# Kernel tuning notes

Hardware: AMD Instinct MI355X
Metric: run time of the kernel (lower is better)

The kernel has to match this reference:

```python
import jax, jax.numpy as jnp
import numpy as np

# ---- static config (mirrors HashEncoderHyFluid.__init__) ----
MIN_RES = np.array([16, 16, 16, 16], dtype=np.float64)
MAX_RES = np.array([256, 256, 256, 128], dtype=np.float64)
NUM_SCALES = 16
MAX_PARAMS = 2 ** 19
F = 2  # features_per_level
N_QUERIES = 1_000_000
PRIMES = np.array([1, 2654435761, 805459861, 3674653429], dtype=np.uint32)
# 16 corner offsets of the 4D hypercube, bit d of idx selects low/high along dim d
BITS = np.array([[(i >> d) & 1 for d in range(4)] for i in range(16)], dtype=np.int32)  # (16,4)


def build_config():
    b = np.exp((np.log(MAX_RES) - np.log(MIN_RES)) / (NUM_SCALES - 1))
    shapes, sizes, indicators, offsets = [], [], [], []
    total = 0
    for s in range(NUM_SCALES):
        res = np.ceil(MIN_RES * np.power(b, s)).astype(np.int64)
        raw = int(res[0] + 1) * int(res[1] + 1) * int(res[2] + 1) * int(res[3] + 1)
        p = raw if raw % 8 == 0 else ((raw + 7) // 8) * 8
        p = min(MAX_PARAMS, p)
        shapes.append(res)
        sizes.append(p)
        indicators.append(1 if raw <= p else 0)
        offsets.append(total)
        total += p * F
    return shapes, sizes, indicators, offsets, total


SHAPES, SIZES, INDICATORS, OFFSETS, TOTAL_HASH_SIZE = build_config()  # total = 15205344


def setup_inputs() -> dict:
    key = jax.random.key(0)
    k1, k2 = jax.random.split(key)
    xyzt = jax.random.uniform(k1, (N_QUERIES, 4), dtype=jnp.float32)  # coords in [0,1)
    hash_table = (jax.random.uniform(k2, (TOTAL_HASH_SIZE,), dtype=jnp.float32) * 2.0 - 1.0) * 0.001
    return {"xyzt": xyzt, "hash_table": hash_table}


def _encode_scale(xyzt, hash_table, res, size, indicator, offset):
    # xyzt: (N,4) in [0,1]; res: np int64 (4,)
    resf = jnp.asarray(res.astype(np.float32))
    pos = xyzt * resf                      # (N,4) grid-space position
    grid = jnp.floor(pos)
    frac = pos - grid                      # (N,4)
    grid = grid.astype(jnp.int32)
    corners = grid[:, None, :] + jnp.asarray(BITS)[None, :, :]          # (N,16,4)
    hi = jnp.asarray(BITS, jnp.float32)[None, :, :]                     # (1,16,4)
    w = jnp.prod(hi * frac[:, None, :] + (1.0 - hi) * (1.0 - frac[:, None, :]), axis=-1)  # (N,16)
    cu = corners.astype(jnp.uint32)
    if indicator == 1:
        # dense linear indexing: strides = cumprod(res+1), wrapping at uint32 like taichi
        strides = np.cumprod(np.concatenate([[1], (res + 1)[:3]])).astype(np.uint32)
        idx = jnp.sum(cu * jnp.asarray(strides), axis=-1)               # (N,16) uint32, wraps
    else:
        # xor hash with large primes
        h = cu[..., 0] * jnp.uint32(PRIMES[0])
        for d in range(1, 4):
            h = h ^ (cu[..., d] * jnp.uint32(PRIMES[d]))
        idx = h
    idx = (idx % jnp.uint32(size)).astype(jnp.int32)
    base = offset + idx * F                                             # (N,16)
    feats = hash_table[base[..., None] + jnp.arange(F)]                 # (N,16,F)
    return jnp.einsum("nc,ncf->nf", w, feats)                           # (N,F)


def reference(xyzt, hash_table):
    outs = []
    for s in range(NUM_SCALES):
        outs.append(_encode_scale(xyzt, hash_table, SHAPES[s], SIZES[s], INDICATORS[s], OFFSETS[s]))
    return jnp.concatenate(outs, axis=-1)  # (N, NUM_SCALES * F)
```

## Files before the change

kernel.cpp:

```cpp
#include <hip/hip_runtime.h>
#include <cstdint>
#include <cmath>


#define NSCALES 16
#define TPB 256

struct Cfg {
  float    res[NSCALES][4];
  uint32_t key[NSCALES][4];
  uint32_t mask[NSCALES];
  int      offset[NSCALES];
  int      dense[NSCALES];
};

typedef float v4f __attribute__((ext_vector_type(4)));
typedef float v2f __attribute__((ext_vector_type(2)));

__global__ __launch_bounds__(TPB) void gather_kernel(
    const float*  __restrict__ xyzt,
    const float*  __restrict__ table,
    float2*       __restrict__ ws,
    int N, Cfg cfg)
{
  const int s = blockIdx.y;
  const int q = blockIdx.x * TPB + threadIdx.x;
  if (q >= N) return;
  const v4f c = __builtin_nontemporal_load(
      reinterpret_cast<const v4f*>(xyzt) + q);

  const float rx = cfg.res[s][0], ry = cfg.res[s][1];
  const float rz = cfg.res[s][2], rw = cfg.res[s][3];
  const uint32_t K0 = cfg.key[s][0], K1 = cfg.key[s][1];
  const uint32_t K2 = cfg.key[s][2], K3 = cfg.key[s][3];

  const float px = c.x * rx, py = c.y * ry, pz = c.z * rz, pw = c.w * rw;
  const float gx = floorf(px), gy = floorf(py), gz = floorf(pz), gw = floorf(pw);
  const float fx = px - gx, fy = py - gy, fz = pz - gz, fw = pw - gw;
  const uint32_t ix = (uint32_t)(int)gx, iy = (uint32_t)(int)gy;
  const uint32_t iz = (uint32_t)(int)gz, iw = (uint32_t)(int)gw;

  const uint32_t x0 = ix * K0, x1 = x0 + K0;
  const uint32_t y0 = iy * K1, y1 = y0 + K1;
  const uint32_t z0 = iz * K2, z1 = z0 + K2;
  const uint32_t u0 = iw * K3, u1 = u0 + K3;

  const float wx0 = 1.f - fx, wy0 = 1.f - fy, wz0 = 1.f - fz, ww0 = 1.f - fw;
  const float wA[4] = { wx0 * wy0, fx * wy0, wx0 * fy, fx * fy };
  const float wB[4] = { wz0 * ww0, fz * ww0, wz0 * fw, fz * fw };

  const float*  tbf = table + cfg.offset[s];
  const float2* __restrict__ tb  = reinterpret_cast<const float2*>(tbf);
  const float4* __restrict__ tb4 = reinterpret_cast<const float4*>(tbf);

  float a0 = 0.f, a1 = 0.f;
  if (cfg.dense[s]) {
    const uint32_t hA[4] = { x0 + y0, x1 + y0, x0 + y1, x1 + y1 };
    const uint32_t hB[4] = { z0 + u0, z1 + u0, z0 + u1, z1 + u1 };
#pragma unroll
    for (int i = 0; i < 16; ++i) {
      const uint32_t idx = hA[i & 3] + hB[i >> 2];
      const float2 v = tb[idx];
      const float w = wA[i & 3] * wB[i >> 2];
      a0 = fmaf(w, v.x, a0);
      a1 = fmaf(w, v.y, a1);
    }
  } else {
    const uint32_t msk = cfg.mask[s];
    if ((ix & 1u) == 0u) {
      const uint32_t yv[2] = { y0, y1 };
      const uint32_t zw[4] = { z0 ^ u0, z1 ^ u0, z0 ^ u1, z1 ^ u1 };
#pragma unroll
      for (int j = 0; j < 8; ++j) {
        const int jy = j & 1, jz = j >> 1;
        const uint32_t p  = (x0 ^ yv[jy] ^ zw[jz]) & msk;
        const uint32_t e  = p & ~1u;
        const uint32_t sel = p & 1u;
        const float4 v = tb4[e >> 1];
        const float wlo = wA[2 * jy]     * wB[jz];
        const float whi = wA[2 * jy + 1] * wB[jz];
        const float l0 = sel ? v.z : v.x, l1 = sel ? v.w : v.y;
        const float h0 = sel ? v.x : v.z, h1 = sel ? v.y : v.w;
        a0 = fmaf(wlo, l0, fmaf(whi, h0, a0));
        a1 = fmaf(wlo, l1, fmaf(whi, h1, a1));
      }
    } else {
      const uint32_t hA[4] = { x0 ^ y0, x1 ^ y0, x0 ^ y1, x1 ^ y1 };
      const uint32_t hB[4] = { z0 ^ u0, z1 ^ u0, z0 ^ u1, z1 ^ u1 };
#pragma unroll
      for (int i = 0; i < 16; ++i) {
        const uint32_t idx = (hA[i & 3] ^ hB[i >> 2]) & msk;
        const float2 v = tb[idx];
        const float w = wA[i & 3] * wB[i >> 2];
        a0 = fmaf(w, v.x, a0);
        a1 = fmaf(w, v.y, a1);
      }
    }
  }
  v2f val = { a0, a1 };
  __builtin_nontemporal_store(val, (v2f*)&ws[(size_t)s * N + q]);
}

__global__ __launch_bounds__(TPB) void transpose_kernel(
    const float2* __restrict__ ws,
    float*        __restrict__ out,
    int N)
{
  __shared__ float2 st[NSCALES][TPB + 1];
  const int t  = threadIdx.x;
  const int q  = blockIdx.x * TPB + t;
  const int ql = q < N ? q : N - 1;

#pragma unroll
  for (int s = 0; s < NSCALES; ++s)
    st[s][t] = ws[(size_t)s * N + ql];

  __syncthreads();

  const int base = blockIdx.x * (TPB * 2 * NSCALES);
#pragma unroll
  for (int it = 0; it < 8; ++it) {
    const int G  = it * 1024 + t * 4;
    const int qi = G >> 5;
    const int s0 = (G & 31) >> 1;
    if (blockIdx.x * TPB + qi < N) {
      const float2 a = st[s0][qi];
      const float2 b = st[s0 + 1][qi];
      v4f val = { a.x, a.y, b.x, b.y };
      __builtin_nontemporal_store(val, (v4f*)(out + base + G));
    }
  }
}

__global__ __launch_bounds__(TPB) void hashenc_fused(
    const float4* __restrict__ xyzt,
    const float*  __restrict__ table,
    float*        __restrict__ out,
    int N, Cfg cfg)
{
  __shared__ float2 st[NSCALES][TPB + 1];
  const int t  = threadIdx.x;
  const int q  = blockIdx.x * TPB + t;
  const int ql = q < N ? q : N - 1;
  const float4 c = xyzt[ql];

#pragma unroll 1
  for (int s = 0; s < NSCALES; ++s) {
    const float rx = cfg.res[s][0], ry = cfg.res[s][1];
    const float rz = cfg.res[s][2], rw = cfg.res[s][3];
    const uint32_t K0 = cfg.key[s][0], K1 = cfg.key[s][1];
    const uint32_t K2 = cfg.key[s][2], K3 = cfg.key[s][3];
    const float px = c.x * rx, py = c.y * ry, pz = c.z * rz, pw = c.w * rw;
    const float gx = floorf(px), gy = floorf(py), gz = floorf(pz), gw = floorf(pw);
    const float fx = px - gx, fy = py - gy, fz = pz - gz, fw = pw - gw;
    const uint32_t ix = (uint32_t)(int)gx, iy = (uint32_t)(int)gy;
    const uint32_t iz = (uint32_t)(int)gz, iw = (uint32_t)(int)gw;
    const uint32_t x0 = ix * K0, x1 = x0 + K0;
    const uint32_t y0 = iy * K1, y1 = y0 + K1;
    const uint32_t z0 = iz * K2, z1 = z0 + K2;
    const uint32_t u0 = iw * K3, u1 = u0 + K3;
    const float wx0 = 1.f - fx, wy0 = 1.f - fy, wz0 = 1.f - fz, ww0 = 1.f - fw;
    const float wA[4] = { wx0 * wy0, fx * wy0, wx0 * fy, fx * fy };
    const float wB[4] = { wz0 * ww0, fz * ww0, wz0 * fw, fz * fw };
    const float2* __restrict__ tb =
        reinterpret_cast<const float2*>(table + cfg.offset[s]);
    float a0 = 0.f, a1 = 0.f;
    if (cfg.dense[s]) {
      const uint32_t hA[4] = { x0 + y0, x1 + y0, x0 + y1, x1 + y1 };
      const uint32_t hB[4] = { z0 + u0, z1 + u0, z0 + u1, z1 + u1 };
#pragma unroll
      for (int i = 0; i < 16; ++i) {
        const uint32_t idx = hA[i & 3] + hB[i >> 2];
        const float2 v = tb[idx];
        const float w = wA[i & 3] * wB[i >> 2];
        a0 = fmaf(w, v.x, a0); a1 = fmaf(w, v.y, a1);
      }
    } else {
      const uint32_t msk = cfg.mask[s];
      const uint32_t hA[4] = { x0 ^ y0, x1 ^ y0, x0 ^ y1, x1 ^ y1 };
      const uint32_t hB[4] = { z0 ^ u0, z1 ^ u0, z0 ^ u1, z1 ^ u1 };
#pragma unroll
      for (int i = 0; i < 16; ++i) {
        const uint32_t idx = (hA[i & 3] ^ hB[i >> 2]) & msk;
        const float2 v = tb[idx];
        const float w = wA[i & 3] * wB[i >> 2];
        a0 = fmaf(w, v.x, a0); a1 = fmaf(w, v.y, a1);
      }
    }
    st[s][t] = make_float2(a0, a1);
  }
  __syncthreads();
  const int base = blockIdx.x * (TPB * 2 * NSCALES);
#pragma unroll
  for (int it = 0; it < 8; ++it) {
    const int G  = it * 1024 + t * 4;
    const int qi = G >> 5;
    const int s0 = (G & 31) >> 1;
    if (blockIdx.x * TPB + qi < N) {
      const float2 a = st[s0][qi];
      const float2 b = st[s0 + 1][qi];
      v4f val = { a.x, a.y, b.x, b.y };
      __builtin_nontemporal_store(val, (v4f*)(out + base + G));
    }
  }
}

static void build_cfg(Cfg& cfg)
{
  const double minr[4] = { 16.0, 16.0, 16.0, 16.0 };
  const double maxr[4] = { 256.0, 256.0, 256.0, 128.0 };
  const uint32_t primes[4] = { 1u, 2654435761u, 805459861u, 3674653429u };

  double b[4];
  for (int d = 0; d < 4; ++d)
    b[d] = ::exp((::log(maxr[d]) - ::log(minr[d])) / (double)(NSCALES - 1));

  long long total = 0;
  for (int s = 0; s < NSCALES; ++s) {
    long long res[4];
    for (int d = 0; d < 4; ++d)
      res[d] = (long long)::ceil(minr[d] * ::pow(b[d], (double)s));

    const long long raw =
        (res[0] + 1) * (res[1] + 1) * (res[2] + 1) * (res[3] + 1);
    long long p = (raw % 8 == 0) ? raw : ((raw + 7) / 8) * 8;
    if (p > 524288) p = 524288;
    const int ind = (raw <= p) ? 1 : 0;

    for (int d = 0; d < 4; ++d) cfg.res[s][d] = (float)res[d];
    if (ind) {
      cfg.key[s][0] = 1u;
      cfg.key[s][1] = (uint32_t)(res[0] + 1);
      cfg.key[s][2] = (uint32_t)((res[0] + 1) * (res[1] + 1));
      cfg.key[s][3] = (uint32_t)((res[0] + 1) * (res[1] + 1) * (res[2] + 1));
    } else {
      for (int d = 0; d < 4; ++d) cfg.key[s][d] = primes[d];
    }
    cfg.mask[s]   = (uint32_t)(p - 1);
    cfg.offset[s] = (int)total;
    cfg.dense[s]  = ind;
    total += p * 2;
  }
}

extern "C" void kernel_launch(void* const* d_in, const int* in_sizes, int n_in,
                              void* d_out, int out_size, void* d_ws, size_t ws_size,
                              hipStream_t stream)
{
  const float*  xyzt  = (const float*)d_in[0];
  const float*  table = (const float*)d_in[1];
  float*        out   = (float*)d_out;
  const int N = in_sizes[0] / 4;

  Cfg cfg;
  build_cfg(cfg);

  const int qblocks = (N + TPB - 1) / TPB;
  const size_t need = (size_t)N * NSCALES * sizeof(float2);

  if (ws_size >= need) {
    float2* ws = (float2*)d_ws;
    hipLaunchKernelGGL(gather_kernel, dim3(qblocks, NSCALES), dim3(TPB), 0,
                       stream, xyzt, table, ws, N, cfg);
    hipLaunchKernelGGL(transpose_kernel, dim3(qblocks), dim3(TPB), 0,
                       stream, ws, out, N);
  } else {
    hipLaunchKernelGGL(hashenc_fused, dim3(qblocks), dim3(TPB), 0,
                       stream, (const float4*)xyzt, table, out, N, cfg);
  }
}
```

Baseline: 876.8 us.

## Bucket-sort queries by Morton key before gathering to improve table locality

Adds a counting-sort pipeline (histogram, single-block scan, atomic scatter) that reorders query coordinates by a 4D Morton bucket key, so neighbouring threads touch nearby hash-table entries in the dense scales. The gather then runs on the sorted coordinates, and a new transpose scatters the results back to the original order through the permutation. This brings extra kernels, atomics, a serial single-block scan and scattered output writes. It also needs more workspace and falls back to the old path when the workspace is too small.

```diff
diff --git a/kernel.cpp b/kernel.cpp
--- a/kernel.cpp
+++ b/kernel.cpp
@@ -5,6 +5,7 @@
 
 #define NSCALES 16
 #define TPB 256
+#define BINS 65536
 
 struct Cfg {
   float    res[NSCALES][4];
@@ -17,8 +18,71 @@
 typedef float v4f __attribute__((ext_vector_type(4)));
 typedef float v2f __attribute__((ext_vector_type(2)));
 
+__device__ __forceinline__ uint32_t bucket_key(float x, float y, float z, float w)
+{
+  uint32_t bx = (uint32_t)(x * 16.f); bx = bx > 15u ? 15u : bx;
+  uint32_t by = (uint32_t)(y * 16.f); by = by > 15u ? 15u : by;
+  uint32_t bz = (uint32_t)(z * 16.f); bz = bz > 15u ? 15u : bz;
+  uint32_t bt = (uint32_t)(w * 16.f); bt = bt > 15u ? 15u : bt;
+  uint32_t k = 0;
+#pragma unroll
+  for (int b = 0; b < 4; ++b) {
+    k |= ((bx >> b) & 1u) << (4 * b + 0);
+    k |= ((by >> b) & 1u) << (4 * b + 1);
+    k |= ((bz >> b) & 1u) << (4 * b + 2);
+    k |= ((bt >> b) & 1u) << (4 * b + 3);
+  }
+  return k;
+}
+
+__global__ __launch_bounds__(TPB) void hist_kernel(
+    const float* __restrict__ xyzt, uint32_t* __restrict__ hist, int N)
+{
+  const int i = blockIdx.x * TPB + threadIdx.x;
+  if (i >= N) return;
+  const v4f c = *(reinterpret_cast<const v4f*>(xyzt) + i);
+  atomicAdd(&hist[bucket_key(c.x, c.y, c.z, c.w)], 1u);
+}
+
+__global__ __launch_bounds__(256) void scan_kernel(
+    const uint32_t* __restrict__ hist, uint32_t* __restrict__ boff)
+{
+  __shared__ uint32_t part[256];
+  const int t = threadIdx.x;
+  const int base = t * (BINS / 256);
+  uint32_t s = 0;
+  for (int j = 0; j < BINS / 256; ++j) s += hist[base + j];
+  part[t] = s;
+  __syncthreads();
+  for (int off = 1; off < 256; off <<= 1) {
+    uint32_t v = (t >= off) ? part[t - off] : 0u;
+    __syncthreads();
+    part[t] += v;
+    __syncthreads();
+  }
+  uint32_t run = part[t] - s;
+  for (int j = 0; j < BINS / 256; ++j) {
+    boff[base + j] = run;
+    run += hist[base + j];
+  }
+}
+
+__global__ __launch_bounds__(TPB) void scatter_kernel(
+    const float* __restrict__ xyzt,
+    const uint32_t* __restrict__ boff, uint32_t* __restrict__ cur,
+    uint32_t* __restrict__ perm, float* __restrict__ c_sorted, int N)
+{
+  const int i = blockIdx.x * TPB + threadIdx.x;
+  if (i >= N) return;
+  const v4f c = *(reinterpret_cast<const v4f*>(xyzt) + i);
+  const uint32_t k = bucket_key(c.x, c.y, c.z, c.w);
+  const uint32_t pos = boff[k] + atomicAdd(&cur[k], 1u);
+  perm[pos] = (uint32_t)i;
+  *(reinterpret_cast<v4f*>(c_sorted) + pos) = c;
+}
+
 __global__ __launch_bounds__(TPB) void gather_kernel(
-    const float*  __restrict__ xyzt,
+    const float*  __restrict__ coords,
     const float*  __restrict__ table,
     float2*       __restrict__ ws,
     int N, Cfg cfg)
@@ -26,8 +90,7 @@
   const int s = blockIdx.y;
   const int q = blockIdx.x * TPB + threadIdx.x;
   if (q >= N) return;
-  const v4f c = __builtin_nontemporal_load(
-      reinterpret_cast<const v4f*>(xyzt) + q);
+  const v4f c = *(reinterpret_cast<const v4f*>(coords) + q);
 
   const float rx = cfg.res[s][0], ry = cfg.res[s][1];
   const float rz = cfg.res[s][2], rw = cfg.res[s][3];
@@ -101,6 +164,24 @@
   __builtin_nontemporal_store(val, (v2f*)&ws[(size_t)s * N + q]);
 }
 
+__global__ __launch_bounds__(TPB) void transpose_direct(
+    const float2*   __restrict__ ws,
+    const uint32_t* __restrict__ perm,
+    float*          __restrict__ out,
+    int N)
+{
+  const int g = blockIdx.x * TPB + threadIdx.x;
+  if (g >= N * 8) return;
+  const int q  = g >> 3;
+  const int l8 = g & 7;
+  const int s0 = l8 * 2;
+  const float2 a = ws[(size_t)s0 * N + q];
+  const float2 b = ws[(size_t)(s0 + 1) * N + q];
+  const uint32_t pq = perm[q];
+  v4f val = { a.x, a.y, b.x, b.y };
+  __builtin_nontemporal_store(val, (v4f*)(out + (size_t)pq * 32 + l8 * 4));
+}
+
 __global__ __launch_bounds__(TPB) void transpose_kernel(
     const float2* __restrict__ ws,
     float*        __restrict__ out,
@@ -110,13 +191,10 @@
   const int t  = threadIdx.x;
   const int q  = blockIdx.x * TPB + t;
   const int ql = q < N ? q : N - 1;
-
 #pragma unroll
   for (int s = 0; s < NSCALES; ++s)
     st[s][t] = ws[(size_t)s * N + ql];
-
   __syncthreads();
-
   const int base = blockIdx.x * (TPB * 2 * NSCALES);
 #pragma unroll
   for (int it = 0; it < 8; ++it) {
@@ -143,7 +221,6 @@
   const int q  = blockIdx.x * TPB + t;
   const int ql = q < N ? q : N - 1;
   const float4 c = xyzt[ql];
-
 #pragma unroll 1
   for (int s = 0; s < NSCALES; ++s) {
     const float rx = cfg.res[s][0], ry = cfg.res[s][1];
@@ -243,22 +320,55 @@
   }
 }
 
+static inline size_t align_up(size_t v, size_t a) { return (v + a - 1) & ~(a - 1); }
+
 extern "C" void kernel_launch(void* const* d_in, const int* in_sizes, int n_in,
                               void* d_out, int out_size, void* d_ws, size_t ws_size,
                               hipStream_t stream)
 {
-  const float*  xyzt  = (const float*)d_in[0];
-  const float*  table = (const float*)d_in[1];
-  float*        out   = (float*)d_out;
+  const float* xyzt  = (const float*)d_in[0];
+  const float* table = (const float*)d_in[1];
+  float*       out   = (float*)d_out;
   const int N = in_sizes[0] / 4;
 
   Cfg cfg;
   build_cfg(cfg);
 
   const int qblocks = (N + TPB - 1) / TPB;
-  const size_t need = (size_t)N * NSCALES * sizeof(float2);
-
-  if (ws_size >= need) {
+
+  size_t off = 0;
+  const size_t perm_off = off;             off = align_up(off + (size_t)N * 4, 256);
+  const size_t hist_off = off;             off = align_up(off + (size_t)BINS * 4, 256);
+  const size_t cur_off  = off;             off = align_up(off + (size_t)BINS * 4, 256);
+  const size_t boff_off = off;             off = align_up(off + (size_t)BINS * 4, 256);
+  const size_t cs_off   = align_up(off, 16);  off = cs_off + (size_t)N * 16;
+  const size_t ws_off   = align_up(off, 16);
+  const size_t need_sorted = ws_off + (size_t)N * NSCALES * sizeof(float2);
+  const size_t need_plain  = (size_t)N * NSCALES * sizeof(float2);
+
+  char* wsb = (char*)d_ws;
+
+  if (ws_size >= need_sorted) {
+    uint32_t* perm = (uint32_t*)(wsb + perm_off);
+    uint32_t* hist = (uint32_t*)(wsb + hist_off);
+    uint32_t* cur  = (uint32_t*)(wsb + cur_off);
+    uint32_t* boff = (uint32_t*)(wsb + boff_off);
+    float*    csrt = (float*)(wsb + cs_off);
+    float2*   ws   = (float2*)(wsb + ws_off);
+
+    hipMemsetAsync(hist, 0, (size_t)BINS * 4, stream);
+    hipMemsetAsync(cur,  0, (size_t)BINS * 4, stream);
+    hipLaunchKernelGGL(hist_kernel, dim3(qblocks), dim3(TPB), 0, stream,
+                       xyzt, hist, N);
+    hipLaunchKernelGGL(scan_kernel, dim3(1), dim3(256), 0, stream, hist, boff);
+    hipLaunchKernelGGL(scatter_kernel, dim3(qblocks), dim3(TPB), 0, stream,
+                       xyzt, boff, cur, perm, csrt, N);
+    hipLaunchKernelGGL(gather_kernel, dim3(qblocks, NSCALES), dim3(TPB), 0,
+                       stream, csrt, table, ws, N, cfg);
+    const int tblocks = (N * 8 + TPB - 1) / TPB;
+    hipLaunchKernelGGL(transpose_direct, dim3(tblocks), dim3(TPB), 0, stream,
+                       ws, perm, out, N);
+  } else if (ws_size >= need_plain) {
     float2* ws = (float2*)d_ws;
     hipLaunchKernelGGL(gather_kernel, dim3(qblocks, NSCALES), dim3(TPB), 0,
                        stream, xyzt, table, ws, N, cfg);
```

Result: faster. 835.6 us (-4.7%).
